# Kernel tuning notes

Hardware: AMD Instinct MI355X
Metric: run time of the kernel (lower is better)

## Reference

```python
import jax, jax.numpy as jnp
import numpy as np

B, D, HID, DC, K = 32768, 64, 512, 128, 12
CLAMP = 1.0
L1 = D // 2          # GLOW split lengths
L2 = D - L1
INIT = 0.01          # torch code rescales all params to 0.01*randn


def setup_inputs() -> dict:
    key = jax.random.key(0)
    ks = iter(jax.random.split(key, 16))
    # FrEIA PermuteRandom: np.random.seed(k); np.random.permutation(D)
    perms = jnp.asarray(
        np.stack([np.random.RandomState(k).permutation(D) for k in range(K)]),
        dtype=jnp.int32)
    f32 = jnp.float32
    return {
        'q_feat': jax.random.normal(next(ks), (B, 1, D), f32),
        'H': jax.random.normal(next(ks), (B, DC), f32),
        'perms': perms,
        'an_logscale': INIT * jax.random.normal(next(ks), (K, D), f32),
        'an_bias': INIT * jax.random.normal(next(ks), (K, D), f32),
        's1_W1': INIT * jax.random.normal(next(ks), (K, HID, L1 + DC), f32),
        's1_b1': INIT * jax.random.normal(next(ks), (K, HID), f32),
        's1_W2': INIT * jax.random.normal(next(ks), (K, 2 * L2, HID), f32),
        's1_b2': INIT * jax.random.normal(next(ks), (K, 2 * L2), f32),
        's2_W1': INIT * jax.random.normal(next(ks), (K, HID, L2 + DC), f32),
        's2_b1': INIT * jax.random.normal(next(ks), (K, HID), f32),
        's2_W2': INIT * jax.random.normal(next(ks), (K, 2 * L1, HID), f32),
        's2_b2': INIT * jax.random.normal(next(ks), (K, 2 * L1), f32),
    }


def _mlp(x, W1, b1, W2, b2):
    # torch Linear: y = x @ W.T + b
    h = jax.nn.relu(x @ W1.T + b1)
    return h @ W2.T + b2


def _log_e(s):
    # FrEIA GLOW soft clamp: log e(s) = clamp * 0.636 * atan(s / clamp)
    return CLAMP * 0.636 * jnp.arctan(s / CLAMP)


def reference(q_feat, H, perms, an_logscale, an_bias,
              s1_W1, s1_b1, s1_W2, s1_b2,
              s2_W1, s2_b1, s2_W2, s2_b2):
    x = q_feat.reshape(q_feat.shape[0], -1)          # Flatten: (B,1,D)->(B,D)
    logj = jnp.zeros(x.shape[0], x.dtype)

    def block(carry, p):
        x, logj = carry
        perm, ls, bi, w11, b11, w12, b12, w21, b21, w22, b22 = p
        x = x[:, perm]                               # PermuteRandom (logdet 0)
        x = x * jnp.exp(ls) + bi                     # ActNorm
        logj = logj + jnp.sum(ls)
        x1, x2 = x[:, :L1], x[:, L1:]                # GLOW coupling
        r2 = _mlp(jnp.concatenate([x2, H], 1), w21, b21, w22, b22)
        le2 = _log_e(r2[:, :L1])
        y1 = jnp.exp(le2) * x1 + r2[:, L1:]
        r1 = _mlp(jnp.concatenate([y1, H], 1), w11, b11, w12, b12)
        le1 = _log_e(r1[:, :L2])
        y2 = jnp.exp(le1) * x2 + r1[:, L2:]
        logj = logj + jnp.sum(le1, axis=1) + jnp.sum(le2, axis=1)
        return (jnp.concatenate([y1, y2], 1), logj), None

    (z, logj), _ = jax.lax.scan(
        block, (x, logj),
        (perms, an_logscale, an_bias,
         s1_W1, s1_b1, s1_W2, s1_b2,
         s2_W1, s2_b1, s2_W2, s2_b2))
    return z, logj
```

## Files before the change

kernel.cpp:

```cpp
#include <hip/hip_runtime.h>
#include <hip/hip_bf16.h>
#include <math.h>

#define B_ROWS 32768

typedef __attribute__((ext_vector_type(8)))  short        s8v;
typedef __attribute__((ext_vector_type(4)))  float        f4v;
typedef __attribute__((ext_vector_type(2)))  unsigned int u2v;
typedef __attribute__((ext_vector_type(4)))  unsigned int u4v;

__device__ __forceinline__ short f2bf(float f){
  unsigned u = __builtin_bit_cast(unsigned, f);
  u = (u + 0x7fffu + ((u >> 16) & 1u)) >> 16;
  return (short)u;
}
__device__ __forceinline__ unsigned cpk(float a, float b){
  __hip_bfloat16_raw lo = (__hip_bfloat16_raw)__float2bfloat16(a);
  __hip_bfloat16_raw hi = (__hip_bfloat16_raw)__float2bfloat16(b);
  return (unsigned)lo.x | ((unsigned)hi.x << 16);
}
__device__ __forceinline__ float bf_lo(unsigned u){ return __builtin_bit_cast(float, u << 16); }
__device__ __forceinline__ float bf_hi(unsigned u){ return __builtin_bit_cast(float, u & 0xffff0000u); }

#define MFMA16(A,B,C) __builtin_amdgcn_mfma_f32_16x16x32_bf16((A),(B),(C),0,0,0)

#define OXFT 0
#define XFT_S 132
#define OHB  33792
#define HB_S 136
#define OW1  68608
#define W1BUF 43008
#define W1_S 168
#define OLJ  154624
#define OPERM 155136
#define OELS 155392
#define OBIV 155648
#define OSLS 155904
#define SM_SZ 155920

#define SL_S 68
#define SLOT_B 17408
#define OSL0 (OW1 + W1BUF)

#define O_S1W1 0
#define O_S1W2 983040
#define O_S2W1 1376256
#define O_S2W2 2359296
#define W_TOTAL 2752512

__global__ void cvtw(const float* __restrict__ s1w1, const float* __restrict__ s1w2,
                     const float* __restrict__ s2w1, const float* __restrict__ s2w2,
                     unsigned short* __restrict__ dst)
{
  long t = (long)blockIdx.x * blockDim.x + threadIdx.x;
  if (t >= W_TOTAL) return;
  float v;
  if      (t < O_S1W2) v = s1w1[t];
  else if (t < O_S2W1) v = s1w2[t - O_S1W2];
  else if (t < O_S2W2) v = s2w1[t - O_S2W1];
  else                 v = s2w2[t - O_S2W2];
  dst[t] = (unsigned short)f2bf(v);
}

template<int USEBF>
__device__ __forceinline__ s8v ldw(const unsigned short* wb, const float* wf, int off){
  if (USEBF){
    return *(const s8v*)(wb + off);
  } else {
    f4v a = *(const f4v*)(wf + off);
    f4v b = *(const f4v*)(wf + off + 4);
    u4v u = {cpk(a[0],a[1]), cpk(a[2],a[3]), cpk(b[0],b[1]), cpk(b[2],b[3])};
    return __builtin_bit_cast(s8v, u);
  }
}

struct MP { const unsigned short* w1b; const float* w1f;
            const unsigned short* w2b; const float* w2f;
            const float* b1; const float* b2; };

__device__ __forceinline__ MP getmp(int m, const unsigned short* wbf,
    const float* s1W1f, const float* s1W2f, const float* s2W1f, const float* s2W2f,
    const float* s1b1, const float* s1b2, const float* s2b1, const float* s2b2)
{
  int blk = m >> 1;
  MP r;
  if (m & 1){
    r.w1b = wbf + O_S1W1 + (size_t)blk*81920; r.w1f = s1W1f + (size_t)blk*81920;
    r.w2b = wbf + O_S1W2 + (size_t)blk*32768; r.w2f = s1W2f + (size_t)blk*32768;
    r.b1 = s1b1 + blk*512; r.b2 = s1b2 + blk*64;
  } else {
    r.w1b = wbf + O_S2W1 + (size_t)blk*81920; r.w1f = s2W1f + (size_t)blk*81920;
    r.w2b = wbf + O_S2W2 + (size_t)blk*32768; r.w2f = s2W2f + (size_t)blk*32768;
    r.b1 = s2b1 + blk*512; r.b2 = s2b2 + blk*64;
  }
  return r;
}

template<int USEBF>
__device__ __forceinline__ void issue_w1(const MP& p, int cchunk, int tid,
                                         u4v wt[5], f4v wtf[10])
{
  if (USEBF){
    const unsigned short* s = p.w1b + cchunk*20480;
    #pragma unroll
    for (int k = 0; k < 5; ++k) wt[k] = *(const u4v*)(s + (size_t)(k*512+tid)*8);
  } else {
    const float* s = p.w1f + cchunk*20480;
    #pragma unroll
    for (int k = 0; k < 10; ++k) wtf[k] = *(const f4v*)(s + (size_t)(k*512+tid)*4);
  }
}

template<int USEBF>
__device__ __forceinline__ void write_w1(char* sm, int buf,
                                         const u4v wt[5], const f4v wtf[10],
                                         const int* wr, const int* wc)
{
  short* W1n = (short*)(sm + OW1 + buf*W1BUF);
  if (USEBF){
    #pragma unroll
    for (int k = 0; k < 5; ++k)
      *(u4v*)(W1n + wr[k]*W1_S + wc[k]*8) = wt[k];
  } else {
    #pragma unroll
    for (int k = 0; k < 10; ++k){
      f4v v = wtf[k];
      *(u2v*)(W1n + wr[k]*W1_S + wc[k]*4) = (u2v){cpk(v[0],v[1]), cpk(v[2],v[3])};
    }
  }
}

template<int USEBF>
__device__ __forceinline__ void load_w2(const MP& p, int c, int hw, int l15, int lq, s8v w2o[4]){
  #pragma unroll
  for (int ot = 0; ot < 4; ++ot)
    w2o[ot] = ldw<USEBF>(p.w2b, p.w2f, (ot*16 + l15)*512 + c*128 + hw*32 + lq*8);
}

template<int USEBF>
__device__ __forceinline__ void mlp_body(char* sm, int tid, int m,
    const MP& cur, const MP& nxt, const s8v hfr[4][4], s8v w2cur[4],
    f4v b1cur[2], f4v b2cur[4], const int* wr, const int* wc)
{
  const int lane = tid & 63, wave = tid >> 6;
  const int hw = wave >> 1, ng = wave & 1;
  const int l15 = lane & 15, lq = lane >> 4;
  const int bp = m & 1;
  float* XFT = (float*)(sm + OXFT);
  short* HB  = (short*)(sm + OHB);
  float* LOGJ= (float*)(sm + OLJ);

  const int xbase = bp ? 0 : 32;
  s8v xk[4];
  #pragma unroll
  for (int nt = 0; nt < 4; ++nt){
    int b = ng*64 + nt*16 + l15;
    const float* xp = XFT + (xbase + lq*8)*XFT_S + b;
    u4v u;
    #pragma unroll
    for (int p = 0; p < 4; ++p)
      u[p] = cpk(xp[(2*p)*XFT_S], xp[(2*p+1)*XFT_S]);
    xk[nt] = __builtin_bit_cast(s8v, u);
  }

  f4v racc[4][4];
  #pragma unroll
  for (int ot = 0; ot < 4; ++ot){
    f4v bv = (f4v){0.f,0.f,0.f,0.f};
    if (hw == 0) bv = b2cur[ot];
    #pragma unroll
    for (int nt = 0; nt < 4; ++nt) racc[ot][nt] = bv;
  }

  #pragma unroll
  for (int c = 0; c < 4; ++c){
    u4v wt[5]; f4v wtf[10];
    const MP& pn = (c < 3) ? cur : nxt;
    const int cn = (c < 3) ? c + 1 : 0;
    issue_w1<USEBF>(pn, cn, tid, wt, wtf);
    f4v b1n0 = *(const f4v*)(pn.b1 + cn*128 + hw*32 + lq*4);
    f4v b1n1 = *(const f4v*)(pn.b1 + cn*128 + hw*32 + 16 + lq*4);
    if (c == 3 && hw == 0){
      #pragma unroll
      for (int ot = 0; ot < 4; ++ot)
        b2cur[ot] = *(const f4v*)(nxt.b2 + ot*16 + lq*4);
    }

    const short* W1c = (const short*)(sm + OW1 + (c&1)*W1BUF);
    f4v acc[2][4];
    #pragma unroll
    for (int mt = 0; mt < 2; ++mt){
      f4v bv = b1cur[mt];
      #pragma unroll
      for (int nt = 0; nt < 4; ++nt) acc[mt][nt] = bv;
    }
    #pragma unroll
    for (int kk = 0; kk < 5; ++kk){
      s8v a0 = *(const s8v*)(W1c + (hw*32 +  0 + l15)*W1_S + kk*32 + lq*8);
      s8v a1 = *(const s8v*)(W1c + (hw*32 + 16 + l15)*W1_S + kk*32 + lq*8);
      #pragma unroll
      for (int nt = 0; nt < 4; ++nt){
        s8v bb = (kk == 0) ? xk[nt] : hfr[nt][kk-1];
        acc[0][nt] = MFMA16(a0, bb, acc[0][nt]);
        acc[1][nt] = MFMA16(a1, bb, acc[1][nt]);
      }
    }
    #pragma unroll
    for (int mt = 0; mt < 2; ++mt)
      #pragma unroll
      for (int nt = 0; nt < 4; ++nt){
        float h0 = fmaxf(acc[mt][nt][0],0.f), h1 = fmaxf(acc[mt][nt][1],0.f);
        float h2 = fmaxf(acc[mt][nt][2],0.f), h3 = fmaxf(acc[mt][nt][3],0.f);
        *(u2v*)(HB + (ng*64 + nt*16 + l15)*HB_S + hw*32 + mt*16 + lq*4) = (u2v){cpk(h0,h1), cpk(h2,h3)};
      }
    #pragma unroll
    for (int nt = 0; nt < 4; ++nt){
      s8v bb = *(const s8v*)(HB + (ng*64 + nt*16 + l15)*HB_S + hw*32 + lq*8);
      #pragma unroll
      for (int ot = 0; ot < 4; ++ot)
        racc[ot][nt] = MFMA16(w2cur[ot], bb, racc[ot][nt]);
    }
    write_w1<USEBF>(sm, cn & 1, wt, wtf, wr, wc);
    b1cur[0] = b1n0; b1cur[1] = b1n1;
    load_w2<USEBF>(pn, cn, hw, l15, lq, w2cur);
    __syncthreads();
  }

  {
    short* SL = (hw < 2) ? (short*)(sm + OSL0 + hw*SLOT_B)
                         : (short*)(sm + OHB + (hw-2)*SLOT_B);
    #pragma unroll
    for (int ot = 0; ot < 4; ++ot)
      #pragma unroll
      for (int nt = 0; nt < 4; ++nt)
        *(u2v*)(SL + (ng*64 + nt*16 + l15)*SL_S + ot*16 + lq*4) =
          (u2v){cpk(racc[ot][nt][0], racc[ot][nt][1]), cpk(racc[ot][nt][2], racc[ot][nt][3])};
  }
  __syncthreads();

  {
    int b = tid & 127, og = tid >> 7;
    float le[8] = {0,0,0,0,0,0,0,0}, ra[8] = {0,0,0,0,0,0,0,0};
    #pragma unroll
    for (int mslot = 0; mslot < 4; ++mslot){
      const short* SL = (mslot < 2) ? (const short*)(sm + OSL0 + mslot*SLOT_B)
                                    : (const short*)(sm + OHB + (mslot-2)*SLOT_B);
      u2v L0 = *(const u2v*)(SL + b*SL_S + og*8);
      u2v L1 = *(const u2v*)(SL + b*SL_S + og*8 + 4);
      u2v R0 = *(const u2v*)(SL + b*SL_S + 32 + og*8);
      u2v R1 = *(const u2v*)(SL + b*SL_S + 32 + og*8 + 4);
      le[0]+=bf_lo(L0[0]); le[1]+=bf_hi(L0[0]); le[2]+=bf_lo(L0[1]); le[3]+=bf_hi(L0[1]);
      le[4]+=bf_lo(L1[0]); le[5]+=bf_hi(L1[0]); le[6]+=bf_lo(L1[1]); le[7]+=bf_hi(L1[1]);
      ra[0]+=bf_lo(R0[0]); ra[1]+=bf_hi(R0[0]); ra[2]+=bf_lo(R0[1]); ra[3]+=bf_hi(R0[1]);
      ra[4]+=bf_lo(R1[0]); ra[5]+=bf_hi(R1[0]); ra[6]+=bf_lo(R1[1]); ra[7]+=bf_hi(R1[1]);
    }
    float part = 0.f;
    #pragma unroll
    for (int j = 0; j < 8; ++j){
      float l = 0.636f * atanf(le[j]);
      int d = bp*32 + og*8 + j;
      float y = __expf(l) * XFT[d*XFT_S + b] + ra[j];
      XFT[d*XFT_S + b] = y;
      part += l;
    }
    atomicAdd(&LOGJ[b], part);
  }
  __syncthreads();
}

template<int USEBF>
__global__ __launch_bounds__(512, 1) void cinn_t(
    const float* __restrict__ q, const float* __restrict__ Hg,
    const int* __restrict__ perms,
    const float* __restrict__ ls_g, const float* __restrict__ bi_g,
    const float* __restrict__ s1b1, const float* __restrict__ s1b2,
    const float* __restrict__ s2b1, const float* __restrict__ s2b2,
    const unsigned short* __restrict__ wbf,
    const float* __restrict__ s1W1f, const float* __restrict__ s1W2f,
    const float* __restrict__ s2W1f, const float* __restrict__ s2W2f,
    float* __restrict__ outz, float* __restrict__ outlj)
{
  __shared__ __align__(16) char sm[SM_SZ];
  const int tid = threadIdx.x;
  const int rowbase = blockIdx.x * 128;
  const int lane = tid & 63, wave = tid >> 6;
  const int hw = wave >> 1, ng = wave & 1;
  const int l15 = lane & 15, lq = lane >> 4;

  float* XFT = (float*)(sm + OXFT);
  float* LOGJ = (float*)(sm + OLJ);
  int*   PERM = (int*)(sm + OPERM);
  float* ELS  = (float*)(sm + OELS);
  float* BIV  = (float*)(sm + OBIV);
  float* SLSp = (float*)(sm + OSLS);

  int wr[10], wc[10];
  if (USEBF){
    #pragma unroll
    for (int k = 0; k < 5; ++k){ int i = k*512 + tid; wr[k] = i/20; wc[k] = i - wr[k]*20; }
  } else {
    #pragma unroll
    for (int k = 0; k < 10; ++k){ int i = k*512 + tid; wr[k] = i/40; wc[k] = i - wr[k]*40; }
  }

  {
    int b = tid >> 2, j = tid & 3;
    const float* src = q + (size_t)(rowbase + b)*64 + j*16;
    #pragma unroll
    for (int i = 0; i < 4; ++i){
      f4v v = *(const f4v*)(src + 4*i);
      #pragma unroll
      for (int jj = 0; jj < 4; ++jj)
        XFT[(j*16 + 4*i + jj)*XFT_S + b] = v[jj];
    }
  }
  if (tid < 128) LOGJ[tid] = 0.f;
  if (tid == 0)  *SLSp = 0.f;
  __syncthreads();
  if (tid < 64){
    float p = 0.f;
    #pragma unroll
    for (int k = 0; k < 12; ++k) p += ls_g[k*64 + tid];
    atomicAdd(SLSp, p);
  }

  s8v hfr[4][4];
  #pragma unroll
  for (int nt = 0; nt < 4; ++nt){
    int b = rowbase + ng*64 + nt*16 + l15;
    #pragma unroll
    for (int kkh = 0; kkh < 4; ++kkh){
      const float* hp = Hg + (size_t)b*128 + kkh*32 + lq*8;
      f4v a = *(const f4v*)hp;
      f4v c = *(const f4v*)(hp + 4);
      u4v u = {cpk(a[0],a[1]), cpk(a[2],a[3]), cpk(c[0],c[1]), cpk(c[2],c[3])};
      hfr[nt][kkh] = __builtin_bit_cast(s8v, u);
    }
  }

  s8v w2cur[4];
  f4v b1cur[2], b2cur[4];
  {
    MP p0 = getmp(0, wbf, s1W1f, s1W2f, s2W1f, s2W2f, s1b1, s1b2, s2b1, s2b2);
    u4v wt[5]; f4v wtf[10];
    issue_w1<USEBF>(p0, 0, tid, wt, wtf);
    write_w1<USEBF>(sm, 0, wt, wtf, wr, wc);
    b1cur[0] = *(const f4v*)(p0.b1 + hw*32 + lq*4);
    b1cur[1] = *(const f4v*)(p0.b1 + hw*32 + 16 + lq*4);
    if (hw == 0){
      #pragma unroll
      for (int ot = 0; ot < 4; ++ot)
        b2cur[ot] = *(const f4v*)(p0.b2 + ot*16 + lq*4);
    }
    load_w2<USEBF>(p0, 0, hw, l15, lq, w2cur);
  }

  for (int m = 0; m < 24; ++m){
    if (!(m & 1)){
      int blk = m >> 1;
      if (tid < 64){
        PERM[tid] = perms[blk*64 + tid];
        ELS[tid]  = __expf(ls_g[blk*64 + tid]);
        BIV[tid]  = bi_g[blk*64 + tid];
      }
      __syncthreads();
      {
        int d = lane, bg = wave;
        int pd = PERM[d];
        f4v v[4];
        #pragma unroll
        for (int i = 0; i < 4; ++i)
          v[i] = *(const f4v*)(XFT + pd*XFT_S + bg*16 + 4*i);
        __syncthreads();
        float e = ELS[d], bi = BIV[d];
        #pragma unroll
        for (int i = 0; i < 4; ++i){
          #pragma unroll
          for (int jj = 0; jj < 4; ++jj) v[i][jj] = fmaf(v[i][jj], e, bi);
          *(f4v*)(XFT + d*XFT_S + bg*16 + 4*i) = v[i];
        }
      }
      __syncthreads();
    }
    MP cur = getmp(m, wbf, s1W1f, s1W2f, s2W1f, s2W2f, s1b1, s1b2, s2b1, s2b2);
    MP nxt = getmp(m < 23 ? m + 1 : 23, wbf, s1W1f, s1W2f, s2W1f, s2W2f, s1b1, s1b2, s2b1, s2b2);
    mlp_body<USEBF>(sm, tid, m, cur, nxt, hfr, w2cur, b1cur, b2cur, wr, wc);
  }

  {
    int b = tid >> 2, j = tid & 3;
    float* dst = outz + (size_t)(rowbase + b)*64 + j*16;
    #pragma unroll
    for (int i = 0; i < 4; ++i){
      f4v w;
      #pragma unroll
      for (int jj = 0; jj < 4; ++jj)
        w[jj] = XFT[(j*16 + 4*i + jj)*XFT_S + b];
      *(f4v*)(dst + 4*i) = w;
    }
  }
  if (tid < 128) outlj[rowbase + tid] = LOGJ[tid] + *SLSp;
}

extern "C" void kernel_launch(void* const* d_in, const int* in_sizes, int n_in,
                              void* d_out, int out_size, void* d_ws, size_t ws_size,
                              hipStream_t stream)
{
  const float* q    = (const float*)d_in[0];
  const float* Hg   = (const float*)d_in[1];
  const int*   perms= (const int*)  d_in[2];
  const float* ls   = (const float*)d_in[3];
  const float* bi   = (const float*)d_in[4];
  const float* s1W1 = (const float*)d_in[5];
  const float* s1b1 = (const float*)d_in[6];
  const float* s1W2 = (const float*)d_in[7];
  const float* s1b2 = (const float*)d_in[8];
  const float* s2W1 = (const float*)d_in[9];
  const float* s2b1 = (const float*)d_in[10];
  const float* s2W2 = (const float*)d_in[11];
  const float* s2b2 = (const float*)d_in[12];
  float* outz  = (float*)d_out;
  float* outlj = outz + (size_t)B_ROWS * 64;

  int usebf = (ws_size >= (size_t)W_TOTAL * 2) ? 1 : 0;
  unsigned short* wbf = (unsigned short*)d_ws;
  if (usebf){
    cvtw<<<2688, 1024, 0, stream>>>(s1W1, s1W2, s2W1, s2W2, wbf);
    cinn_t<1><<<256, 512, 0, stream>>>(q, Hg, perms, ls, bi,
                                       s1b1, s1b2, s2b1, s2b2,
                                       wbf, s1W1, s1W2, s2W1, s2W2,
                                       outz, outlj);
  } else {
    cinn_t<0><<<256, 512, 0, stream>>>(q, Hg, perms, ls, bi,
                                       s1b1, s1b2, s2b1, s2b2,
                                       wbf, s1W1, s1W2, s2W1, s2W2,
                                       outz, outlj);
  }
}
```

Baseline: 308.7 us.

## Halve rows per block, single-buffer W1 in LDS, run two blocks per CU

Each block now handles 64 rows with 256 threads instead of 128 rows with 512, and LDS shrinks to about 79KB by dropping the W1 double buffer. That lets two blocks share a CU (launch bounds 256,2). W2 and bias loads are no longer prefetched a chunk ahead; they are loaded inside each chunk, and W1 staging now costs an extra barrier per chunk. The aim is latency hiding across co-resident blocks, but each block fetches the full weight set for only half as many rows, so global weight traffic doubles.

```diff
diff --git a/kernel.cpp b/kernel.cpp
--- a/kernel.cpp
+++ b/kernel.cpp
@@ -25,22 +25,20 @@
 #define MFMA16(A,B,C) __builtin_amdgcn_mfma_f32_16x16x32_bf16((A),(B),(C),0,0,0)
 
 #define OXFT 0
-#define XFT_S 132
-#define OHB  33792
-#define HB_S 136
-#define OW1  68608
-#define W1BUF 43008
-#define W1_S 168
-#define OLJ  154624
-#define OPERM 155136
-#define OELS 155392
-#define OBIV 155648
-#define OSLS 155904
-#define SM_SZ 155920
-
-#define SL_S 68
-#define SLOT_B 17408
-#define OSL0 (OW1 + W1BUF)
+#define XFT_S 68
+#define OHB   17408
+#define HB_S  136
+#define OW1   34816
+#define W1_S  168
+#define OSL   OW1
+#define SL_S  68
+#define SLOT_B 8704
+#define OLJ   77824
+#define OPERM 78080
+#define OELS  78336
+#define OBIV  78592
+#define OSLS  78848
+#define SM_SZ 78864
 
 #define O_S1W1 0
 #define O_S1W2 983040
@@ -98,32 +96,32 @@
 
 template<int USEBF>
 __device__ __forceinline__ void issue_w1(const MP& p, int cchunk, int tid,
-                                         u4v wt[5], f4v wtf[10])
+                                         u4v wt[10], f4v wtf[20])
 {
   if (USEBF){
     const unsigned short* s = p.w1b + cchunk*20480;
     #pragma unroll
-    for (int k = 0; k < 5; ++k) wt[k] = *(const u4v*)(s + (size_t)(k*512+tid)*8);
+    for (int k = 0; k < 10; ++k) wt[k] = *(const u4v*)(s + (size_t)(k*256+tid)*8);
   } else {
     const float* s = p.w1f + cchunk*20480;
     #pragma unroll
-    for (int k = 0; k < 10; ++k) wtf[k] = *(const f4v*)(s + (size_t)(k*512+tid)*4);
+    for (int k = 0; k < 20; ++k) wtf[k] = *(const f4v*)(s + (size_t)(k*256+tid)*4);
   }
 }
 
 template<int USEBF>
-__device__ __forceinline__ void write_w1(char* sm, int buf,
-                                         const u4v wt[5], const f4v wtf[10],
+__device__ __forceinline__ void write_w1(char* sm,
+                                         const u4v wt[10], const f4v wtf[20],
                                          const int* wr, const int* wc)
 {
-  short* W1n = (short*)(sm + OW1 + buf*W1BUF);
+  short* W1n = (short*)(sm + OW1);
   if (USEBF){
     #pragma unroll
-    for (int k = 0; k < 5; ++k)
+    for (int k = 0; k < 10; ++k)
       *(u4v*)(W1n + wr[k]*W1_S + wc[k]*8) = wt[k];
   } else {
     #pragma unroll
-    for (int k = 0; k < 10; ++k){
+    for (int k = 0; k < 20; ++k){
       f4v v = wtf[k];
       *(u2v*)(W1n + wr[k]*W1_S + wc[k]*4) = (u2v){cpk(v[0],v[1]), cpk(v[2],v[3])};
     }
@@ -131,145 +129,7 @@
 }
 
 template<int USEBF>
-__device__ __forceinline__ void load_w2(const MP& p, int c, int hw, int l15, int lq, s8v w2o[4]){
-  #pragma unroll
-  for (int ot = 0; ot < 4; ++ot)
-    w2o[ot] = ldw<USEBF>(p.w2b, p.w2f, (ot*16 + l15)*512 + c*128 + hw*32 + lq*8);
-}
-
-template<int USEBF>
-__device__ __forceinline__ void mlp_body(char* sm, int tid, int m,
-    const MP& cur, const MP& nxt, const s8v hfr[4][4], s8v w2cur[4],
-    f4v b1cur[2], f4v b2cur[4], const int* wr, const int* wc)
-{
-  const int lane = tid & 63, wave = tid >> 6;
-  const int hw = wave >> 1, ng = wave & 1;
-  const int l15 = lane & 15, lq = lane >> 4;
-  const int bp = m & 1;
-  float* XFT = (float*)(sm + OXFT);
-  short* HB  = (short*)(sm + OHB);
-  float* LOGJ= (float*)(sm + OLJ);
-
-  const int xbase = bp ? 0 : 32;
-  s8v xk[4];
-  #pragma unroll
-  for (int nt = 0; nt < 4; ++nt){
-    int b = ng*64 + nt*16 + l15;
-    const float* xp = XFT + (xbase + lq*8)*XFT_S + b;
-    u4v u;
-    #pragma unroll
-    for (int p = 0; p < 4; ++p)
-      u[p] = cpk(xp[(2*p)*XFT_S], xp[(2*p+1)*XFT_S]);
-    xk[nt] = __builtin_bit_cast(s8v, u);
-  }
-
-  f4v racc[4][4];
-  #pragma unroll
-  for (int ot = 0; ot < 4; ++ot){
-    f4v bv = (f4v){0.f,0.f,0.f,0.f};
-    if (hw == 0) bv = b2cur[ot];
-    #pragma unroll
-    for (int nt = 0; nt < 4; ++nt) racc[ot][nt] = bv;
-  }
-
-  #pragma unroll
-  for (int c = 0; c < 4; ++c){
-    u4v wt[5]; f4v wtf[10];
-    const MP& pn = (c < 3) ? cur : nxt;
-    const int cn = (c < 3) ? c + 1 : 0;
-    issue_w1<USEBF>(pn, cn, tid, wt, wtf);
-    f4v b1n0 = *(const f4v*)(pn.b1 + cn*128 + hw*32 + lq*4);
-    f4v b1n1 = *(const f4v*)(pn.b1 + cn*128 + hw*32 + 16 + lq*4);
-    if (c == 3 && hw == 0){
-      #pragma unroll
-      for (int ot = 0; ot < 4; ++ot)
-        b2cur[ot] = *(const f4v*)(nxt.b2 + ot*16 + lq*4);
-    }
-
-    const short* W1c = (const short*)(sm + OW1 + (c&1)*W1BUF);
-    f4v acc[2][4];
-    #pragma unroll
-    for (int mt = 0; mt < 2; ++mt){
-      f4v bv = b1cur[mt];
-      #pragma unroll
-      for (int nt = 0; nt < 4; ++nt) acc[mt][nt] = bv;
-    }
-    #pragma unroll
-    for (int kk = 0; kk < 5; ++kk){
-      s8v a0 = *(const s8v*)(W1c + (hw*32 +  0 + l15)*W1_S + kk*32 + lq*8);
-      s8v a1 = *(const s8v*)(W1c + (hw*32 + 16 + l15)*W1_S + kk*32 + lq*8);
-      #pragma unroll
-      for (int nt = 0; nt < 4; ++nt){
-        s8v bb = (kk == 0) ? xk[nt] : hfr[nt][kk-1];
-        acc[0][nt] = MFMA16(a0, bb, acc[0][nt]);
-        acc[1][nt] = MFMA16(a1, bb, acc[1][nt]);
-      }
-    }
-    #pragma unroll
-    for (int mt = 0; mt < 2; ++mt)
-      #pragma unroll
-      for (int nt = 0; nt < 4; ++nt){
-        float h0 = fmaxf(acc[mt][nt][0],0.f), h1 = fmaxf(acc[mt][nt][1],0.f);
-        float h2 = fmaxf(acc[mt][nt][2],0.f), h3 = fmaxf(acc[mt][nt][3],0.f);
-        *(u2v*)(HB + (ng*64 + nt*16 + l15)*HB_S + hw*32 + mt*16 + lq*4) = (u2v){cpk(h0,h1), cpk(h2,h3)};
-      }
-    #pragma unroll
-    for (int nt = 0; nt < 4; ++nt){
-      s8v bb = *(const s8v*)(HB + (ng*64 + nt*16 + l15)*HB_S + hw*32 + lq*8);
-      #pragma unroll
-      for (int ot = 0; ot < 4; ++ot)
-        racc[ot][nt] = MFMA16(w2cur[ot], bb, racc[ot][nt]);
-    }
-    write_w1<USEBF>(sm, cn & 1, wt, wtf, wr, wc);
-    b1cur[0] = b1n0; b1cur[1] = b1n1;
-    load_w2<USEBF>(pn, cn, hw, l15, lq, w2cur);
-    __syncthreads();
-  }
-
-  {
-    short* SL = (hw < 2) ? (short*)(sm + OSL0 + hw*SLOT_B)
-                         : (short*)(sm + OHB + (hw-2)*SLOT_B);
-    #pragma unroll
-    for (int ot = 0; ot < 4; ++ot)
-      #pragma unroll
-      for (int nt = 0; nt < 4; ++nt)
-        *(u2v*)(SL + (ng*64 + nt*16 + l15)*SL_S + ot*16 + lq*4) =
-          (u2v){cpk(racc[ot][nt][0], racc[ot][nt][1]), cpk(racc[ot][nt][2], racc[ot][nt][3])};
-  }
-  __syncthreads();
-
-  {
-    int b = tid & 127, og = tid >> 7;
-    float le[8] = {0,0,0,0,0,0,0,0}, ra[8] = {0,0,0,0,0,0,0,0};
-    #pragma unroll
-    for (int mslot = 0; mslot < 4; ++mslot){
-      const short* SL = (mslot < 2) ? (const short*)(sm + OSL0 + mslot*SLOT_B)
-                                    : (const short*)(sm + OHB + (mslot-2)*SLOT_B);
-      u2v L0 = *(const u2v*)(SL + b*SL_S + og*8);
-      u2v L1 = *(const u2v*)(SL + b*SL_S + og*8 + 4);
-      u2v R0 = *(const u2v*)(SL + b*SL_S + 32 + og*8);
-      u2v R1 = *(const u2v*)(SL + b*SL_S + 32 + og*8 + 4);
-      le[0]+=bf_lo(L0[0]); le[1]+=bf_hi(L0[0]); le[2]+=bf_lo(L0[1]); le[3]+=bf_hi(L0[1]);
-      le[4]+=bf_lo(L1[0]); le[5]+=bf_hi(L1[0]); le[6]+=bf_lo(L1[1]); le[7]+=bf_hi(L1[1]);
-      ra[0]+=bf_lo(R0[0]); ra[1]+=bf_hi(R0[0]); ra[2]+=bf_lo(R0[1]); ra[3]+=bf_hi(R0[1]);
-      ra[4]+=bf_lo(R1[0]); ra[5]+=bf_hi(R1[0]); ra[6]+=bf_lo(R1[1]); ra[7]+=bf_hi(R1[1]);
-    }
-    float part = 0.f;
-    #pragma unroll
-    for (int j = 0; j < 8; ++j){
-      float l = 0.636f * atanf(le[j]);
-      int d = bp*32 + og*8 + j;
-      float y = __expf(l) * XFT[d*XFT_S + b] + ra[j];
-      XFT[d*XFT_S + b] = y;
-      part += l;
-    }
-    atomicAdd(&LOGJ[b], part);
-  }
-  __syncthreads();
-}
-
-template<int USEBF>
-__global__ __launch_bounds__(512, 1) void cinn_t(
+__global__ __launch_bounds__(256, 2) void cinn_t(
     const float* __restrict__ q, const float* __restrict__ Hg,
     const int* __restrict__ perms,
     const float* __restrict__ ls_g, const float* __restrict__ bi_g,
@@ -282,25 +142,26 @@
 {
   __shared__ __align__(16) char sm[SM_SZ];
   const int tid = threadIdx.x;
-  const int rowbase = blockIdx.x * 128;
-  const int lane = tid & 63, wave = tid >> 6;
-  const int hw = wave >> 1, ng = wave & 1;
+  const int rowbase = blockIdx.x * 64;
+  const int lane = tid & 63;
+  const int hw = tid >> 6;
   const int l15 = lane & 15, lq = lane >> 4;
 
   float* XFT = (float*)(sm + OXFT);
-  float* LOGJ = (float*)(sm + OLJ);
-  int*   PERM = (int*)(sm + OPERM);
-  float* ELS  = (float*)(sm + OELS);
-  float* BIV  = (float*)(sm + OBIV);
-  float* SLSp = (float*)(sm + OSLS);
-
-  int wr[10], wc[10];
+  short* HB  = (short*)(sm + OHB);
+  float* LOGJ= (float*)(sm + OLJ);
+  int*   PERM= (int*)(sm + OPERM);
+  float* ELS = (float*)(sm + OELS);
+  float* BIV = (float*)(sm + OBIV);
+  float* SLSp= (float*)(sm + OSLS);
+
+  int wr[20], wc[20];
   if (USEBF){
     #pragma unroll
-    for (int k = 0; k < 5; ++k){ int i = k*512 + tid; wr[k] = i/20; wc[k] = i - wr[k]*20; }
-  } else {
-    #pragma unroll
-    for (int k = 0; k < 10; ++k){ int i = k*512 + tid; wr[k] = i/40; wc[k] = i - wr[k]*40; }
+    for (int k = 0; k < 10; ++k){ int i = k*256 + tid; wr[k] = i/20; wc[k] = i - wr[k]*20; }
+  } else {
+    #pragma unroll
+    for (int k = 0; k < 20; ++k){ int i = k*256 + tid; wr[k] = i/40; wc[k] = i - wr[k]*40; }
   }
 
   {
@@ -314,8 +175,8 @@
         XFT[(j*16 + 4*i + jj)*XFT_S + b] = v[jj];
     }
   }
-  if (tid < 128) LOGJ[tid] = 0.f;
-  if (tid == 0)  *SLSp = 0.f;
+  if (tid < 64) LOGJ[tid] = 0.f;
+  if (tid == 0) *SLSp = 0.f;
   __syncthreads();
   if (tid < 64){
     float p = 0.f;
@@ -327,7 +188,7 @@
   s8v hfr[4][4];
   #pragma unroll
   for (int nt = 0; nt < 4; ++nt){
-    int b = rowbase + ng*64 + nt*16 + l15;
+    int b = rowbase + nt*16 + l15;
     #pragma unroll
     for (int kkh = 0; kkh < 4; ++kkh){
       const float* hp = Hg + (size_t)b*128 + kkh*32 + lq*8;
@@ -338,25 +199,20 @@
     }
   }
 
-  s8v w2cur[4];
-  f4v b1cur[2], b2cur[4];
+  u4v wt[10]; f4v wtf[20];
   {
     MP p0 = getmp(0, wbf, s1W1f, s1W2f, s2W1f, s2W2f, s1b1, s1b2, s2b1, s2b2);
-    u4v wt[5]; f4v wtf[10];
     issue_w1<USEBF>(p0, 0, tid, wt, wtf);
-    write_w1<USEBF>(sm, 0, wt, wtf, wr, wc);
-    b1cur[0] = *(const f4v*)(p0.b1 + hw*32 + lq*4);
-    b1cur[1] = *(const f4v*)(p0.b1 + hw*32 + 16 + lq*4);
-    if (hw == 0){
-      #pragma unroll
-      for (int ot = 0; ot < 4; ++ot)
-        b2cur[ot] = *(const f4v*)(p0.b2 + ot*16 + lq*4);
-    }
-    load_w2<USEBF>(p0, 0, hw, l15, lq, w2cur);
-  }
+    write_w1<USEBF>(sm, wt, wtf, wr, wc);
+  }
+  __syncthreads();
 
   for (int m = 0; m < 24; ++m){
-    if (!(m & 1)){
+    const int bp = m & 1;
+    MP cur = getmp(m, wbf, s1W1f, s1W2f, s2W1f, s2W2f, s1b1, s1b2, s2b1, s2b2);
+    MP nxt = getmp(m < 23 ? m + 1 : 23, wbf, s1W1f, s1W2f, s2W1f, s2W2f, s1b1, s1b2, s2b1, s2b2);
+
+    if (!bp){
       int blk = m >> 1;
       if (tid < 64){
         PERM[tid] = perms[blk*64 + tid];
@@ -365,7 +221,7 @@
       }
       __syncthreads();
       {
-        int d = lane, bg = wave;
+        int d = lane, bg = hw;
         int pd = PERM[d];
         f4v v[4];
         #pragma unroll
@@ -382,9 +238,135 @@
       }
       __syncthreads();
     }
-    MP cur = getmp(m, wbf, s1W1f, s1W2f, s2W1f, s2W2f, s1b1, s1b2, s2b1, s2b2);
-    MP nxt = getmp(m < 23 ? m + 1 : 23, wbf, s1W1f, s1W2f, s2W1f, s2W2f, s1b1, s1b2, s2b1, s2b2);
-    mlp_body<USEBF>(sm, tid, m, cur, nxt, hfr, w2cur, b1cur, b2cur, wr, wc);
+
+    const int xbase = bp ? 0 : 32;
+    s8v xk[4];
+    #pragma unroll
+    for (int nt = 0; nt < 4; ++nt){
+      int b = nt*16 + l15;
+      const float* xp = XFT + (xbase + lq*8)*XFT_S + b;
+      u4v u;
+      #pragma unroll
+      for (int p = 0; p < 4; ++p)
+        u[p] = cpk(xp[(2*p)*XFT_S], xp[(2*p+1)*XFT_S]);
+      xk[nt] = __builtin_bit_cast(s8v, u);
+    }
+
+    f4v b2v[4];
+    if (hw == 0){
+      #pragma unroll
+      for (int ot = 0; ot < 4; ++ot)
+        b2v[ot] = *(const f4v*)(cur.b2 + ot*16 + lq*4);
+    }
+
+    f4v racc[4][4];
+    #pragma unroll
+    for (int ot = 0; ot < 4; ++ot)
+      #pragma unroll
+      for (int nt = 0; nt < 4; ++nt)
+        racc[ot][nt] = (f4v){0.f,0.f,0.f,0.f};
+
+    #pragma unroll
+    for (int c = 0; c < 4; ++c){
+      const MP& pn = (c < 3) ? cur : nxt;
+      const int cn = (c < 3) ? c + 1 : 0;
+      if (!(m == 23 && c == 3)) issue_w1<USEBF>(pn, cn, tid, wt, wtf);
+      s8v w2c[4];
+      #pragma unroll
+      for (int ot = 0; ot < 4; ++ot)
+        w2c[ot] = ldw<USEBF>(cur.w2b, cur.w2f, (ot*16 + l15)*512 + c*128 + hw*32 + lq*8);
+      f4v b1v0 = *(const f4v*)(cur.b1 + c*128 + hw*32 + lq*4);
+      f4v b1v1 = *(const f4v*)(cur.b1 + c*128 + hw*32 + 16 + lq*4);
+
+      const short* W1c = (const short*)(sm + OW1);
+      f4v acc[2][4];
+      #pragma unroll
+      for (int mt = 0; mt < 2; ++mt)
+        #pragma unroll
+        for (int nt = 0; nt < 4; ++nt) acc[mt][nt] = (f4v){0.f,0.f,0.f,0.f};
+      #pragma unroll
+      for (int kk = 0; kk < 5; ++kk){
+        s8v a0 = *(const s8v*)(W1c + (hw*32 +  0 + l15)*W1_S + kk*32 + lq*8);
+        s8v a1 = *(const s8v*)(W1c + (hw*32 + 16 + l15)*W1_S + kk*32 + lq*8);
+        #pragma unroll
+        for (int nt = 0; nt < 4; ++nt){
+          s8v bb = (kk == 0) ? xk[nt] : hfr[nt][kk-1];
+          acc[0][nt] = MFMA16(a0, bb, acc[0][nt]);
+          acc[1][nt] = MFMA16(a1, bb, acc[1][nt]);
+        }
+      }
+      #pragma unroll
+      for (int mt = 0; mt < 2; ++mt){
+        f4v bv = mt ? b1v1 : b1v0;
+        #pragma unroll
+        for (int nt = 0; nt < 4; ++nt){
+          float h0 = fmaxf(acc[mt][nt][0] + bv[0], 0.f);
+          float h1 = fmaxf(acc[mt][nt][1] + bv[1], 0.f);
+          float h2 = fmaxf(acc[mt][nt][2] + bv[2], 0.f);
+          float h3 = fmaxf(acc[mt][nt][3] + bv[3], 0.f);
+          *(u2v*)(HB + (nt*16 + l15)*HB_S + hw*32 + mt*16 + lq*4) = (u2v){cpk(h0,h1), cpk(h2,h3)};
+        }
+      }
+      #pragma unroll
+      for (int nt = 0; nt < 4; ++nt){
+        s8v bb = *(const s8v*)(HB + (nt*16 + l15)*HB_S + hw*32 + lq*8);
+        #pragma unroll
+        for (int ot = 0; ot < 4; ++ot)
+          racc[ot][nt] = MFMA16(w2c[ot], bb, racc[ot][nt]);
+      }
+      __syncthreads();
+      if (c < 3){
+        write_w1<USEBF>(sm, wt, wtf, wr, wc);
+        __syncthreads();
+      }
+    }
+
+    {
+      short* SL = (short*)(sm + OSL + hw*SLOT_B);
+      #pragma unroll
+      for (int ot = 0; ot < 4; ++ot)
+        #pragma unroll
+        for (int nt = 0; nt < 4; ++nt){
+          float r0 = racc[ot][nt][0], r1 = racc[ot][nt][1];
+          float r2 = racc[ot][nt][2], r3 = racc[ot][nt][3];
+          if (hw == 0){ r0 += b2v[ot][0]; r1 += b2v[ot][1]; r2 += b2v[ot][2]; r3 += b2v[ot][3]; }
+          *(u2v*)(SL + (nt*16 + l15)*SL_S + ot*16 + lq*4) = (u2v){cpk(r0,r1), cpk(r2,r3)};
+        }
+    }
+    __syncthreads();
+
+    {
+      int b = tid & 63, og = tid >> 6;
+      float le[8] = {0,0,0,0,0,0,0,0}, ra[8] = {0,0,0,0,0,0,0,0};
+      #pragma unroll
+      for (int ms = 0; ms < 4; ++ms){
+        const short* SL = (const short*)(sm + OSL + ms*SLOT_B);
+        u2v L0 = *(const u2v*)(SL + b*SL_S + og*8);
+        u2v L1 = *(const u2v*)(SL + b*SL_S + og*8 + 4);
+        u2v R0 = *(const u2v*)(SL + b*SL_S + 32 + og*8);
+        u2v R1 = *(const u2v*)(SL + b*SL_S + 32 + og*8 + 4);
+        le[0]+=bf_lo(L0[0]); le[1]+=bf_hi(L0[0]); le[2]+=bf_lo(L0[1]); le[3]+=bf_hi(L0[1]);
+        le[4]+=bf_lo(L1[0]); le[5]+=bf_hi(L1[0]); le[6]+=bf_lo(L1[1]); le[7]+=bf_hi(L1[1]);
+        ra[0]+=bf_lo(R0[0]); ra[1]+=bf_hi(R0[0]); ra[2]+=bf_lo(R0[1]); ra[3]+=bf_hi(R0[1]);
+        ra[4]+=bf_lo(R1[0]); ra[5]+=bf_hi(R1[0]); ra[6]+=bf_lo(R1[1]); ra[7]+=bf_hi(R1[1]);
+      }
+      float part = 0.f;
+      #pragma unroll
+      for (int j = 0; j < 8; ++j){
+        float l = 0.636f * atanf(le[j]);
+        int d = bp*32 + og*8 + j;
+        float y = __expf(l) * XFT[d*XFT_S + b] + ra[j];
+        XFT[d*XFT_S + b] = y;
+        part += l;
+      }
+      atomicAdd(&LOGJ[b], part);
+    }
+    __syncthreads();
+
+    if (m < 23){
+      write_w1<USEBF>(sm, wt, wtf, wr, wc);
+      __syncthreads();
+    }
   }
 
   {
@@ -399,7 +381,7 @@
       *(f4v*)(dst + 4*i) = w;
     }
   }
-  if (tid < 128) outlj[rowbase + tid] = LOGJ[tid] + *SLSp;
+  if (tid < 64) outlj[rowbase + tid] = LOGJ[tid] + *SLSp;
 }
 
 extern "C" void kernel_launch(void* const* d_in, const int* in_sizes, int n_in,
@@ -426,12 +408,12 @@
   unsigned short* wbf = (unsigned short*)d_ws;
   if (usebf){
     cvtw<<<2688, 1024, 0, stream>>>(s1W1, s1W2, s2W1, s2W2, wbf);
-    cinn_t<1><<<256, 512, 0, stream>>>(q, Hg, perms, ls, bi,
+    cinn_t<1><<<512, 256, 0, stream>>>(q, Hg, perms, ls, bi,
                                        s1b1, s1b2, s2b1, s2b2,
                                        wbf, s1W1, s1W2, s2W1, s2W2,
                                        outz, outlj);
   } else {
-    cinn_t<0><<<256, 512, 0, stream>>>(q, Hg, perms, ls, bi,
+    cinn_t<0><<<512, 256, 0, stream>>>(q, Hg, perms, ls, bi,
                                        s1b1, s1b2, s2b1, s2b2,
                                        wbf, s1W1, s1W2, s2W1, s2W2,
                                        outz, outlj);
```

After: 597.6 us. 1.94x slower.
